# Kernel tuning notes

Measured on AMD Instinct MI355X. Metric: run time of the kernel, lower is better.

The kernel has to match this reference:

```python
import jax, jax.numpy as jnp
import numpy as np

MAX_NUM_CAPS = 10
NEG = -1e9

def _layernorm(x, g, b):
    m = x.mean(-1, keepdims=True)
    v = x.var(-1, keepdims=True)
    return (x - m) / jnp.sqrt(v + 1e-5) * g + b

def _gatv2(x, Wl, Wr, att, bias, adj):
    # x: [B,M,F]; Wl/Wr: [F,H*C]; att: [H,C]; adj: [B,M,M] bool, adj[b,i,j] = edge i->j
    B, M, F = x.shape
    H, C = att.shape
    xl = jnp.einsum('bmf,fhc->bmhc', x, Wl.reshape(F, H, C))  # source transform
    xr = jnp.einsum('bmf,fhc->bmhc', x, Wr.reshape(F, H, C))  # target transform
    # GATv2 score: att . leaky_relu(xl[i] + xr[j]) for edge (src=i, dst=j)
    z = jax.nn.leaky_relu(xl[:, :, None, :, :] + xr[:, None, :, :, :], 0.2)  # [B,i,j,H,C]
    e = jnp.einsum('bijhc,hc->bijh', z, att)
    e = jnp.where(adj[..., None], e, NEG)
    alpha = jax.nn.softmax(e, axis=1)  # softmax over incoming sources i per target j
    out = jnp.einsum('bijh,bihc->bjhc', alpha, xl)  # aggregate at targets
    return out.reshape(B, M, H * C) + bias

def setup_inputs() -> dict:
    key = jax.random.key(0)
    ks = jax.random.split(key, 16)
    B, N, T = 128, 16, 48
    Fm, H, C3 = 128, 4, 64
    s = 0.05
    inp = {
        'team_obs': jax.random.normal(ks[0], (B, N, 14), jnp.float32),
        'target_obs': jax.random.normal(ks[1], (B, T, 15), jnp.float32),
        'team_mask': jax.random.normal(ks[2], (B, 2, N), jnp.float32),
        'local_target_mask': jnp.ones((B, T + 1), jnp.float32),
        'W_emb': jax.random.normal(ks[3], (16, Fm), jnp.float32) * s,
        'b_emb': jnp.zeros((Fm,), jnp.float32),
        'Wl1': jax.random.normal(ks[4], (Fm, Fm), jnp.float32) * s,
        'Wr1': jax.random.normal(ks[5], (Fm, Fm), jnp.float32) * s,
        'att1': jax.random.normal(ks[6], (H, Fm // H), jnp.float32) * s,
        'b1': jnp.zeros((Fm,), jnp.float32),
        'Wl2': jax.random.normal(ks[7], (Fm, Fm), jnp.float32) * s,
        'Wr2': jax.random.normal(ks[8], (Fm, Fm), jnp.float32) * s,
        'att2': jax.random.normal(ks[9], (H, Fm // H), jnp.float32) * s,
        'b2': jnp.zeros((Fm,), jnp.float32),
        'Wl3': jax.random.normal(ks[10], (Fm, C3), jnp.float32) * s,
        'Wr3': jax.random.normal(ks[11], (Fm, C3), jnp.float32) * s,
        'att3': jax.random.normal(ks[12], (1, C3), jnp.float32) * s,
        'b3': jnp.zeros((C3,), jnp.float32),
        'ln1_g': jnp.ones((Fm,), jnp.float32),
        'ln1_b': jnp.zeros((Fm,), jnp.float32),
        'ln2_g': jnp.ones((Fm,), jnp.float32),
        'ln2_b': jnp.zeros((Fm,), jnp.float32),
    }
    return inp

def reference(team_obs, target_obs, team_mask, local_target_mask,
              W_emb, b_emb, Wl1, Wr1, att1, b1, Wl2, Wr2, att2, b2,
              Wl3, Wr3, att3, b3, ln1_g, ln1_b, ln2_g, ln2_b):
    B, N, _ = team_obs.shape
    team = jnp.concatenate([team_obs, jnp.zeros((B, N, 2), team_obs.dtype)], axis=2)
    tgt = target_obs[:, :, :-1]
    T = tgt.shape[1]
    tgt = jnp.concatenate([tgt[:, :, :2 + MAX_NUM_CAPS],
                           jnp.zeros((B, T, 2), tgt.dtype),
                           tgt[:, :, -2:]], axis=2)
    fin = jnp.concatenate([team, tgt], axis=1)  # [B, M, inp_dim]
    h = fin @ W_emb + b_emb  # [B, M, 128]
    imp_team = team_mask[:, 0] != -1e9          # [B, N]
    imp_tgt = local_target_mask[:, :-1] != 0.0  # [B, T]
    imp = jnp.concatenate([imp_team, imp_tgt], axis=1)  # [B, M]
    M = N + T
    eye = jnp.eye(M, dtype=bool)
    # edges among active nodes minus diagonal; PyG GATv2Conv add_self_loops=True re-adds self edges
    adj = (imp[:, :, None] & imp[:, None, :] & ~eye) | eye  # [B, M, M]
    out = jax.nn.relu(_layernorm(_gatv2(h, Wl1, Wr1, att1, b1, adj), ln1_g, ln1_b))
    out = jax.nn.relu(_layernorm(_gatv2(out, Wl2, Wr2, att2, b2, adj), ln2_g, ln2_b))
    out = _gatv2(out, Wl3, Wr3, att3, b3, adj)
    return out  # [B, M, out_dim]
```

## Files before the change

### kernel.cpp

```cpp
#include <hip/hip_runtime.h>

typedef unsigned short u16;
typedef unsigned int   u32;
typedef _Float16 h2  __attribute__((ext_vector_type(2)));
typedef __fp16   hw2 __attribute__((ext_vector_type(2)));
typedef __fp16   hw8 __attribute__((ext_vector_type(8)));
typedef float    f4  __attribute__((ext_vector_type(4)));

#define XS 136

static __device__ __forceinline__ h2 pk(float a, float b) {
    return __builtin_bit_cast(h2, __builtin_amdgcn_cvt_pkrtz(a, b));
}
static __device__ __forceinline__ float dot2(h2 a, h2 b, float c) {
    return __builtin_amdgcn_fdot2(__builtin_bit_cast(hw2, a),
                                  __builtin_bit_cast(hw2, b), c, false);
}
static __device__ __forceinline__ h2  b2h(u32 v) { return __builtin_bit_cast(h2, v); }
static __device__ __forceinline__ u32 h2u(h2 v)  { return __builtin_bit_cast(u32, v); }
static __device__ __forceinline__ h2  abs2(h2 v) { return b2h(h2u(v) & 0x7fff7fffu); }
static __device__ __forceinline__ u16 f2h(float f) { return __builtin_bit_cast(u16, (_Float16)f); }
static __device__ __forceinline__ float h2f(u16 v) { return (float)__builtin_bit_cast(_Float16, v); }
static __device__ __forceinline__ f4 mfma16(uint4 a, uint4 b, f4 c) {
    return __builtin_amdgcn_mfma_f32_16x16x32_f16(__builtin_bit_cast(hw8, a),
                                                  __builtin_bit_cast(hw8, b), c, 0, 0, 0);
}

__global__ void pack_weights(const float* __restrict__ Wl1, const float* __restrict__ Wr1,
                             const float* __restrict__ Wl2, const float* __restrict__ Wr2,
                             const float* __restrict__ Wl3, const float* __restrict__ Wr3,
                             u32* __restrict__ wpk)
{
    const int o = blockIdx.x * 256 + threadIdx.x;
    const float* src; u32* dst; int local; int N;
    if      (o < 8192)  { src = Wl1; dst = wpk;         local = o;         N = 128; }
    else if (o < 16384) { src = Wr1; dst = wpk + 8192;  local = o - 8192;  N = 128; }
    else if (o < 24576) { src = Wl2; dst = wpk + 16384; local = o - 16384; N = 128; }
    else if (o < 32768) { src = Wr2; dst = wpk + 24576; local = o - 24576; N = 128; }
    else if (o < 36864) { src = Wl3; dst = wpk + 32768; local = o - 32768; N = 64;  }
    else                { src = Wr3; dst = wpk + 36864; local = o - 36864; N = 64;  }
    const int i2   = local & 3;
    const int lane = (local >> 2) & 63;
    const int frag = local >> 8;
    const int kb   = frag & 3;
    const int nt   = frag >> 2;
    const int k0   = kb*32 + ((lane >> 4) << 3) + i2*2;
    const int n    = nt*16 + (lane & 15);
    dst[local] = h2u(pk(src[k0*N + n], src[(k0+1)*N + n]));
}

static __device__ __forceinline__ void compute_imp(int t, int b,
    const float* __restrict__ team_mask, const float* __restrict__ ltm, float* sImp)
{
    if (t < 64) {
        float im;
        if (t < 16) im = (team_mask[b*32 + t] != -1000000000.0f) ? 1.f : 0.f;
        else        im = (ltm[b*49 + (t-16)] != 0.0f) ? 1.f : 0.f;
        sImp[t] = im;
    }
}

static __device__ __forceinline__ void matmul128(int w, int lane,
    const u32* __restrict__ wpkL, const u32* __restrict__ wpkR,
    const u16* sX, u16* sXl, uint4* sXrP)
{
    const int  mt  = w & 3;
    const bool isR = (w >= 4);
    const u32* wp  = isR ? wpkR : wpkL;
    const int  n15 = lane & 15;
    const int  qd  = lane >> 4;
    uint4 afr[4];
#pragma unroll
    for (int kb = 0; kb < 4; kb++)
        afr[kb] = *(const uint4*)&sX[(mt*16 + n15)*XS + kb*32 + (qd << 3)];
#pragma unroll
    for (int nt = 0; nt < 8; nt++) {
        f4 acc = {0.f, 0.f, 0.f, 0.f};
#pragma unroll
        for (int kb = 0; kb < 4; kb++) {
            uint4 bf = *(const uint4*)&wp[((nt*4 + kb)*64 + lane)*4];
            acc = mfma16(afr[kb], bf, acc);
        }
        const int n  = nt*16 + n15;
        const int mb = mt*16 + (qd << 2);
        if (!isR) {
#pragma unroll
            for (int r = 0; r < 4; r++) sXl[(mb + r)*XS + n] = f2h(acc[r]);
        } else {
            u16* xp = (u16*)sXrP;
#pragma unroll
            for (int r = 0; r < 4; r++)
                xp[(((n >> 3)*64) + mb + r)*8 + (n & 7)] = f2h(acc[r]);
        }
    }
}

static __device__ __forceinline__ void attn_ln_fused(int w, int lane,
    const float* __restrict__ att, const float* __restrict__ bias,
    const float* __restrict__ lg, const float* __restrict__ lb,
    u16* sXout, const u16* sXl, const uint4* sXrP,
    float* sAl, float* sPart, float* sL2, const float* sImp, u32* sOv)
{
    const int h  = w & 3;
    const int hf = w >> 2;
    const int j  = lane;

    h2 a2[16];
#pragma unroll
    for (int q = 0; q < 16; q++) a2[q] = pk(att[h*32 + 2*q], att[h*32 + 2*q + 1]);

    if (w < 4) {
        const uint4* pr = (const uint4*)&sXl[lane*XS + h*32];
        float al = 0.f;
#pragma unroll
        for (int c4 = 0; c4 < 4; c4++) {
            uint4 v = pr[c4];
            al = dot2(b2h(v.x), a2[c4*4+0], al);
            al = dot2(b2h(v.y), a2[c4*4+1], al);
            al = dot2(b2h(v.z), a2[c4*4+2], al);
            al = dot2(b2h(v.w), a2[c4*4+3], al);
        }
        sAl[h*64 + lane] = al;
    }

    h2 xr2[16];
#pragma unroll
    for (int s = 0; s < 4; s++) {
        uint4 v = sXrP[(h*4 + s)*64 + j];
        xr2[s*4+0] = b2h(v.x); xr2[s*4+1] = b2h(v.y);
        xr2[s*4+2] = b2h(v.z); xr2[s*4+3] = b2h(v.w);
    }
    float Ar = 0.f;
#pragma unroll
    for (int q = 0; q < 16; q++) Ar = dot2(a2[q], xr2[q], Ar);
    const float impj = sImp[j];
    __syncthreads();

    float l = 0.f;
    h2 acc2[16];
#pragma unroll
    for (int q = 0; q < 16; q++) acc2[q] = b2h(0u);
    const int i0 = hf*32;
#pragma unroll 4
    for (int ii = 0; ii < 32; ii++) {
        const int i = i0 + ii;
        const uint4* pl = (const uint4*)&sXl[i*XS + h*32];
        uint4 v0 = pl[0], v1 = pl[1], v2 = pl[2], v3 = pl[3];
        h2 xl2[16];
        xl2[0] = b2h(v0.x); xl2[1] = b2h(v0.y); xl2[2]  = b2h(v0.z); xl2[3]  = b2h(v0.w);
        xl2[4] = b2h(v1.x); xl2[5] = b2h(v1.y); xl2[6]  = b2h(v1.z); xl2[7]  = b2h(v1.w);
        xl2[8] = b2h(v2.x); xl2[9] = b2h(v2.y); xl2[10] = b2h(v2.z); xl2[11] = b2h(v2.w);
        xl2[12]= b2h(v3.x); xl2[13]= b2h(v3.y); xl2[14] = b2h(v3.z); xl2[15] = b2h(v3.w);
        float S0 = 0.f, S1 = 0.f;
#pragma unroll
        for (int q = 0; q < 16; q += 2) {
            h2 t0 = abs2(xl2[q]   + xr2[q]);
            h2 t1 = abs2(xl2[q+1] + xr2[q+1]);
            S0 = dot2(a2[q],   t0, S0);
            S1 = dot2(a2[q+1], t1, S1);
        }
        float e  = 0.6f*(sAl[h*64 + i] + Ar) + 0.4f*(S0 + S1);
        float ad = (i == j) ? 1.f : impj * sImp[i];
        float p  = (ad != 0.f) ? __expf(e) : 0.f;
        l += p;
        h2 p2 = pk(p, p);
#pragma unroll
        for (int q = 0; q < 16; q++) acc2[q] += p2 * xl2[q];
    }

    if (hf == 1) {
        uint4* d4 = (uint4*)(sOv + (h*64 + j)*20);
        uint4 o;
        o.x = h2u(acc2[0]);  o.y = h2u(acc2[1]);  o.z = h2u(acc2[2]);  o.w = h2u(acc2[3]);  d4[0] = o;
        o.x = h2u(acc2[4]);  o.y = h2u(acc2[5]);  o.z = h2u(acc2[6]);  o.w = h2u(acc2[7]);  d4[1] = o;
        o.x = h2u(acc2[8]);  o.y = h2u(acc2[9]);  o.z = h2u(acc2[10]); o.w = h2u(acc2[11]); d4[2] = o;
        o.x = h2u(acc2[12]); o.y = h2u(acc2[13]); o.z = h2u(acc2[14]); o.w = h2u(acc2[15]); d4[3] = o;
        sL2[h*64 + j] = l;
    }
    __syncthreads();

    float yv[32];
    if (hf == 0) {
        const uint4* s4 = (const uint4*)(sOv + (h*64 + j)*20);
        uint4 u0 = s4[0], u1 = s4[1], u2 = s4[2], u3 = s4[3];
        h2 oth[16];
        oth[0] = b2h(u0.x); oth[1] = b2h(u0.y); oth[2]  = b2h(u0.z); oth[3]  = b2h(u0.w);
        oth[4] = b2h(u1.x); oth[5] = b2h(u1.y); oth[6]  = b2h(u1.z); oth[7]  = b2h(u1.w);
        oth[8] = b2h(u2.x); oth[9] = b2h(u2.y); oth[10] = b2h(u2.z); oth[11] = b2h(u2.w);
        oth[12]= b2h(u3.x); oth[13]= b2h(u3.y); oth[14] = b2h(u3.z); oth[15] = b2h(u3.w);
        l += sL2[h*64 + j];
        const float rl = 1.f / l;
        float s1 = 0.f, s2v = 0.f;
#pragma unroll
        for (int q = 0; q < 16; q++) {
            h2 sum = acc2[q] + oth[q];
            float y0 = fmaf((float)sum[0], rl, bias[h*32 + 2*q]);
            float y1 = fmaf((float)sum[1], rl, bias[h*32 + 2*q + 1]);
            yv[2*q] = y0; yv[2*q+1] = y1;
            s1 += y0 + y1;
            s2v = fmaf(y0, y0, s2v);
            s2v = fmaf(y1, y1, s2v);
        }
        sPart[h*64 + j]       = s1;
        sPart[256 + h*64 + j] = s2v;
    }
    __syncthreads();

    if (hf == 0) {
        float su = sPart[j] + sPart[64 + j] + sPart[128 + j] + sPart[192 + j];
        float sq = sPart[256 + j] + sPart[320 + j] + sPart[384 + j] + sPart[448 + j];
        const float mean = su * 0.0078125f;
        const float var  = sq * 0.0078125f - mean*mean;
        const float rstd = rsqrtf(var + 1e-5f);
        u32 orow[16];
#pragma unroll
        for (int q = 0; q < 16; q++) {
            int f0 = h*32 + 2*q;
            float v0 = fmaxf(fmaf((yv[2*q]   - mean)*rstd, lg[f0],   lb[f0]),   0.f);
            float v1 = fmaxf(fmaf((yv[2*q+1] - mean)*rstd, lg[f0+1], lb[f0+1]), 0.f);
            orow[q] = h2u(pk(v0, v1));
        }
        uint4* po = (uint4*)&sXout[j*XS + h*32];
        po[0] = *(uint4*)&orow[0];
        po[1] = *(uint4*)&orow[4];
        po[2] = *(uint4*)&orow[8];
        po[3] = *(uint4*)&orow[12];
    }
}

__global__ void __launch_bounds__(512, 1) gnn_fused(
    const float* __restrict__ team_obs, const float* __restrict__ target_obs,
    const float* __restrict__ team_mask, const float* __restrict__ ltm,
    const float* __restrict__ W_emb, const float* __restrict__ b_emb,
    const float* __restrict__ att1, const float* __restrict__ b1,
    const float* __restrict__ ln1_g, const float* __restrict__ ln1_b,
    const float* __restrict__ att2, const float* __restrict__ b2,
    const float* __restrict__ ln2_g, const float* __restrict__ ln2_b,
    const float* __restrict__ att3, const float* __restrict__ b3,
    const u32* __restrict__ wpk, float* __restrict__ out)
{
    __shared__ __align__(16) u16   sX  [64*XS];
    __shared__ __align__(16) u16   sXl [64*XS];
    __shared__ __align__(16) uint4 sXrP[1024];
    __shared__ float sFin[1024];
    __shared__ float sAl [256];
    __shared__ float sPart[512];
    __shared__ float sL2 [256];
    __shared__ float sImp[64];
    __shared__ __align__(16) u32 sOv[5120];

    const int t    = threadIdx.x;
    const int w    = t >> 6;
    const int lane = t & 63;
    const int b    = blockIdx.x;

    compute_imp(t, b, team_mask, ltm, sImp);
    for (int ee = t; ee < 1024; ee += 512) {
        int m = ee >> 4, k = ee & 15;
        float v = 0.f;
        if (m < 16) {
            if (k < 14) v = team_obs[(b*16 + m)*14 + k];
        } else {
            const float* tg = target_obs + (size_t)(b*48 + (m-16))*15;
            if      (k < 12)  v = tg[k];
            else if (k == 14) v = tg[12];
            else if (k == 15) v = tg[13];
        }
        sFin[m*16 + k] = v;
    }
    __syncthreads();

    {
        const int f = t & 127;
        const int g = t >> 7;
        float wreg[16];
#pragma unroll
        for (int k = 0; k < 16; k++) wreg[k] = W_emb[k*128 + f];
        const float bf = b_emb[f];
#pragma unroll
        for (int mm = 0; mm < 16; mm++) {
            int m = g*16 + mm;
            const float4* pf = (const float4*)&sFin[m*16];
            float4 f0 = pf[0], f1 = pf[1], f2 = pf[2], f3 = pf[3];
            float acc = bf;
            acc = fmaf(f0.x, wreg[0],  acc); acc = fmaf(f0.y, wreg[1],  acc);
            acc = fmaf(f0.z, wreg[2],  acc); acc = fmaf(f0.w, wreg[3],  acc);
            acc = fmaf(f1.x, wreg[4],  acc); acc = fmaf(f1.y, wreg[5],  acc);
            acc = fmaf(f1.z, wreg[6],  acc); acc = fmaf(f1.w, wreg[7],  acc);
            acc = fmaf(f2.x, wreg[8],  acc); acc = fmaf(f2.y, wreg[9],  acc);
            acc = fmaf(f2.z, wreg[10], acc); acc = fmaf(f2.w, wreg[11], acc);
            acc = fmaf(f3.x, wreg[12], acc); acc = fmaf(f3.y, wreg[13], acc);
            acc = fmaf(f3.z, wreg[14], acc); acc = fmaf(f3.w, wreg[15], acc);
            sX[m*XS + f] = f2h(acc);
        }
    }
    __syncthreads();

    matmul128(w, lane, wpk, wpk + 8192, sX, sXl, sXrP);
    __syncthreads();
    attn_ln_fused(w, lane, att1, b1, ln1_g, ln1_b,
                  sX, sXl, sXrP, sAl, sPart, sL2, sImp, sOv);
    __syncthreads();

    matmul128(w, lane, wpk + 16384, wpk + 24576, sX, sXl, sXrP);
    __syncthreads();
    attn_ln_fused(w, lane, att2, b2, ln2_g, ln2_b,
                  sX, sXl, sXrP, sAl, sPart, sL2, sImp, sOv);
    __syncthreads();

    {
        const int  mt  = w & 3;
        const bool isR = (w >= 4);
        const u32* wp  = isR ? (wpk + 36864) : (wpk + 32768);
        const int  n15 = lane & 15;
        const int  qd  = lane >> 4;
        uint4 afr[4];
#pragma unroll
        for (int kb = 0; kb < 4; kb++)
            afr[kb] = *(const uint4*)&sX[(mt*16 + n15)*XS + kb*32 + (qd << 3)];
#pragma unroll
        for (int nt = 0; nt < 4; nt++) {
            f4 acc = {0.f, 0.f, 0.f, 0.f};
#pragma unroll
            for (int kb = 0; kb < 4; kb++) {
                uint4 bf = *(const uint4*)&wp[((nt*4 + kb)*64 + lane)*4];
                acc = mfma16(afr[kb], bf, acc);
            }
            const int n  = nt*16 + n15;
            const int mb = mt*16 + (qd << 2);
            if (!isR) {
#pragma unroll
                for (int r = 0; r < 4; r++) sXl[(mb + r)*XS + n] = f2h(acc[r]);
            } else {
                u16* xp = (u16*)sXrP;
#pragma unroll
                for (int r = 0; r < 4; r++)
                    xp[(((n >> 3)*64) + mb + r)*8 + (n & 7)] = f2h(acc[r]);
            }
        }
    }
    __syncthreads();

    {
        h2 a2l[4];
#pragma unroll
        for (int q = 0; q < 4; q++) a2l[q] = pk(att3[w*8 + 2*q], att3[w*8 + 2*q + 1]);
        uint4 v = *(const uint4*)&sXl[lane*XS + w*8];
        float al = 0.f;
        al = dot2(b2h(v.x), a2l[0], al);
        al = dot2(b2h(v.y), a2l[1], al);
        al = dot2(b2h(v.z), a2l[2], al);
        al = dot2(b2h(v.w), a2l[3], al);
        sPart[w*64 + lane] = al;
    }
    __syncthreads();
    if (t < 64) {
        sAl[t] = ((sPart[t] + sPart[64+t]) + (sPart[128+t] + sPart[192+t]))
               + ((sPart[256+t] + sPart[320+t]) + (sPart[384+t] + sPart[448+t]));
    }
    __syncthreads();

    u16* sE = (u16*)sOv;

    {
        h2 a3[32], xr3[32];
#pragma unroll
        for (int q = 0; q < 32; q++) a3[q] = pk(att3[2*q], att3[2*q + 1]);
#pragma unroll
        for (int s = 0; s < 8; s++) {
            uint4 v = sXrP[s*64 + lane];
            xr3[s*4+0] = b2h(v.x); xr3[s*4+1] = b2h(v.y);
            xr3[s*4+2] = b2h(v.z); xr3[s*4+3] = b2h(v.w);
        }
        float Ar = 0.f;
#pragma unroll
        for (int q = 0; q < 32; q++) Ar = dot2(a3[q], xr3[q], Ar);
        const float impj = sImp[lane];
#pragma unroll
        for (int ii = 0; ii < 8; ii++) {
            const int i = w*8 + ii;
            const uint4* pl = (const uint4*)&sXl[i*XS];
            float S0 = 0.f, S1 = 0.f;
#pragma unroll
            for (int c4 = 0; c4 < 8; c4++) {
                uint4 v = pl[c4];
                S0 = dot2(a3[c4*4+0], abs2(b2h(v.x) + xr3[c4*4+0]), S0);
                S1 = dot2(a3[c4*4+1], abs2(b2h(v.y) + xr3[c4*4+1]), S1);
                S0 = dot2(a3[c4*4+2], abs2(b2h(v.z) + xr3[c4*4+2]), S0);
                S1 = dot2(a3[c4*4+3], abs2(b2h(v.w) + xr3[c4*4+3]), S1);
            }
            float e  = 0.6f*(sAl[i] + Ar) + 0.4f*(S0 + S1);
            float ad = (i == lane) ? 1.f : impj * sImp[i];
            e = (ad != 0.f) ? e : -60000.0f;
            sE[i*64 + lane] = f2h(e);
        }
    }
    __syncthreads();

    {
        const int c0 = w*8;
        h2 acc2[4];
#pragma unroll
        for (int q = 0; q < 4; q++) acc2[q] = b2h(0u);
        float l = 0.f;
        for (int i = 0; i < 64; i++) {
            float p = __expf(h2f(sE[i*64 + lane]));
            l += p;
            h2 p2 = pk(p, p);
            uint4 v = *(const uint4*)&sXl[i*XS + c0];
            acc2[0] += p2 * b2h(v.x);
            acc2[1] += p2 * b2h(v.y);
            acc2[2] += p2 * b2h(v.z);
            acc2[3] += p2 * b2h(v.w);
        }
        const float rl = 1.f / l;
        float o[8];
#pragma unroll
        for (int q = 0; q < 4; q++) {
            o[2*q]   = fmaf((float)acc2[q][0], rl, b3[c0 + 2*q]);
            o[2*q+1] = fmaf((float)acc2[q][1], rl, b3[c0 + 2*q + 1]);
        }
        float4* po = (float4*)(out + (size_t)b*4096 + (size_t)lane*64 + c0);
        po[0] = *(const float4*)&o[0];
        po[1] = *(const float4*)&o[4];
    }
}

extern "C" void kernel_launch(void* const* d_in, const int* in_sizes, int n_in,
                              void* d_out, int out_size, void* d_ws, size_t ws_size,
                              hipStream_t stream) {
    (void)in_sizes; (void)n_in; (void)ws_size; (void)out_size;
    const float* team_obs          = (const float*)d_in[0];
    const float* target_obs        = (const float*)d_in[1];
    const float* team_mask         = (const float*)d_in[2];
    const float* local_target_mask = (const float*)d_in[3];
    const float* W_emb             = (const float*)d_in[4];
    const float* b_emb             = (const float*)d_in[5];
    const float* Wl1               = (const float*)d_in[6];
    const float* Wr1               = (const float*)d_in[7];
    const float* att1              = (const float*)d_in[8];
    const float* b1                = (const float*)d_in[9];
    const float* Wl2               = (const float*)d_in[10];
    const float* Wr2               = (const float*)d_in[11];
    const float* att2              = (const float*)d_in[12];
    const float* b2                = (const float*)d_in[13];
    const float* Wl3               = (const float*)d_in[14];
    const float* Wr3               = (const float*)d_in[15];
    const float* att3              = (const float*)d_in[16];
    const float* b3                = (const float*)d_in[17];
    const float* ln1_g             = (const float*)d_in[18];
    const float* ln1_b             = (const float*)d_in[19];
    const float* ln2_g             = (const float*)d_in[20];
    const float* ln2_b             = (const float*)d_in[21];
    float* out = (float*)d_out;

    u32* wpk = (u32*)d_ws;

    pack_weights<<<dim3(160), dim3(256), 0, stream>>>(Wl1, Wr1, Wl2, Wr2, Wl3, Wr3, wpk);
    gnn_fused<<<dim3(128), dim3(512), 0, stream>>>(
        team_obs, target_obs, team_mask, local_target_mask, W_emb, b_emb,
        att1, b1, ln1_g, ln1_b, att2, b2, ln2_g, ln2_b, att3, b3, wpk, out);
}
```

Before: 146.4 us.

## Double block to 1024 threads and split every stage across 16 waves

The fused GNN kernel now launches 1024 threads per block instead of 512, and each stage splits its work across 16 waves. Matmul N-tiles are halved per wave, the attention source loop is split into four quarters with a three-way shared-memory reduction, and the layer-3 stages use 4 columns per wave. With only 128 blocks on a GPU with many CUs, the aim is more latency hiding per CU. In exchange it uses more shared memory for the partial sums, adds reduction overhead, accumulates in fp32 rather than fp16 when combining partials, and lowers the register budget per thread.

```diff
diff --git a/kernel.cpp b/kernel.cpp
--- a/kernel.cpp
+++ b/kernel.cpp
@@ -65,7 +65,8 @@
     const u16* sX, u16* sXl, uint4* sXrP)
 {
     const int  mt  = w & 3;
-    const bool isR = (w >= 4);
+    const bool isR = (w >> 2) & 1;
+    const int  nh  = w >> 3;
     const u32* wp  = isR ? wpkR : wpkL;
     const int  n15 = lane & 15;
     const int  qd  = lane >> 4;
@@ -74,7 +75,7 @@
     for (int kb = 0; kb < 4; kb++)
         afr[kb] = *(const uint4*)&sX[(mt*16 + n15)*XS + kb*32 + (qd << 3)];
 #pragma unroll
-    for (int nt = 0; nt < 8; nt++) {
+    for (int nt = nh*4; nt < nh*4 + 4; nt++) {
         f4 acc = {0.f, 0.f, 0.f, 0.f};
 #pragma unroll
         for (int kb = 0; kb < 4; kb++) {
@@ -102,7 +103,7 @@
     float* sAl, float* sPart, float* sL2, const float* sImp, u32* sOv)
 {
     const int h  = w & 3;
-    const int hf = w >> 2;
+    const int qf = w >> 2;
     const int j  = lane;
 
     h2 a2[16];
@@ -140,9 +141,9 @@
     h2 acc2[16];
 #pragma unroll
     for (int q = 0; q < 16; q++) acc2[q] = b2h(0u);
-    const int i0 = hf*32;
+    const int i0 = qf*16;
 #pragma unroll 4
-    for (int ii = 0; ii < 32; ii++) {
+    for (int ii = 0; ii < 16; ii++) {
         const int i = i0 + ii;
         const uint4* pl = (const uint4*)&sXl[i*XS + h*32];
         uint4 v0 = pl[0], v1 = pl[1], v2 = pl[2], v3 = pl[3];
@@ -168,45 +169,53 @@
         for (int q = 0; q < 16; q++) acc2[q] += p2 * xl2[q];
     }
 
-    if (hf == 1) {
-        uint4* d4 = (uint4*)(sOv + (h*64 + j)*20);
+    if (qf != 0) {
+        uint4* d4 = (uint4*)(sOv + ((qf-1)*256 + h*64 + j)*20);
         uint4 o;
         o.x = h2u(acc2[0]);  o.y = h2u(acc2[1]);  o.z = h2u(acc2[2]);  o.w = h2u(acc2[3]);  d4[0] = o;
         o.x = h2u(acc2[4]);  o.y = h2u(acc2[5]);  o.z = h2u(acc2[6]);  o.w = h2u(acc2[7]);  d4[1] = o;
         o.x = h2u(acc2[8]);  o.y = h2u(acc2[9]);  o.z = h2u(acc2[10]); o.w = h2u(acc2[11]); d4[2] = o;
         o.x = h2u(acc2[12]); o.y = h2u(acc2[13]); o.z = h2u(acc2[14]); o.w = h2u(acc2[15]); d4[3] = o;
-        sL2[h*64 + j] = l;
-    }
-    __syncthreads();
-
-    float yv[32];
-    if (hf == 0) {
-        const uint4* s4 = (const uint4*)(sOv + (h*64 + j)*20);
-        uint4 u0 = s4[0], u1 = s4[1], u2 = s4[2], u3 = s4[3];
-        h2 oth[16];
-        oth[0] = b2h(u0.x); oth[1] = b2h(u0.y); oth[2]  = b2h(u0.z); oth[3]  = b2h(u0.w);
-        oth[4] = b2h(u1.x); oth[5] = b2h(u1.y); oth[6]  = b2h(u1.z); oth[7]  = b2h(u1.w);
-        oth[8] = b2h(u2.x); oth[9] = b2h(u2.y); oth[10] = b2h(u2.z); oth[11] = b2h(u2.w);
-        oth[12]= b2h(u3.x); oth[13]= b2h(u3.y); oth[14] = b2h(u3.z); oth[15] = b2h(u3.w);
-        l += sL2[h*64 + j];
+        sL2[(qf-1)*256 + h*64 + j] = l;
+    }
+    __syncthreads();
+
+    float fy[32];
+    if (qf == 0) {
+#pragma unroll
+        for (int q = 0; q < 16; q++) {
+            fy[2*q]   = (float)acc2[q][0];
+            fy[2*q+1] = (float)acc2[q][1];
+        }
+#pragma unroll
+        for (int bb = 0; bb < 3; bb++) {
+            const uint4* s4 = (const uint4*)(sOv + (bb*256 + h*64 + j)*20);
+            uint4 U[4];
+            U[0] = s4[0]; U[1] = s4[1]; U[2] = s4[2]; U[3] = s4[3];
+            const u32* uv = (const u32*)U;
+#pragma unroll
+            for (int q = 0; q < 16; q++) {
+                h2 o = b2h(uv[q]);
+                fy[2*q]   += (float)o[0];
+                fy[2*q+1] += (float)o[1];
+            }
+            l += sL2[bb*256 + h*64 + j];
+        }
         const float rl = 1.f / l;
         float s1 = 0.f, s2v = 0.f;
 #pragma unroll
-        for (int q = 0; q < 16; q++) {
-            h2 sum = acc2[q] + oth[q];
-            float y0 = fmaf((float)sum[0], rl, bias[h*32 + 2*q]);
-            float y1 = fmaf((float)sum[1], rl, bias[h*32 + 2*q + 1]);
-            yv[2*q] = y0; yv[2*q+1] = y1;
-            s1 += y0 + y1;
-            s2v = fmaf(y0, y0, s2v);
-            s2v = fmaf(y1, y1, s2v);
+        for (int k = 0; k < 32; k++) {
+            float y = fmaf(fy[k], rl, bias[h*32 + k]);
+            fy[k] = y;
+            s1  += y;
+            s2v  = fmaf(y, y, s2v);
         }
         sPart[h*64 + j]       = s1;
         sPart[256 + h*64 + j] = s2v;
     }
     __syncthreads();
 
-    if (hf == 0) {
+    if (qf == 0) {
         float su = sPart[j] + sPart[64 + j] + sPart[128 + j] + sPart[192 + j];
         float sq = sPart[256 + j] + sPart[320 + j] + sPart[384 + j] + sPart[448 + j];
         const float mean = su * 0.0078125f;
@@ -216,8 +225,8 @@
 #pragma unroll
         for (int q = 0; q < 16; q++) {
             int f0 = h*32 + 2*q;
-            float v0 = fmaxf(fmaf((yv[2*q]   - mean)*rstd, lg[f0],   lb[f0]),   0.f);
-            float v1 = fmaxf(fmaf((yv[2*q+1] - mean)*rstd, lg[f0+1], lb[f0+1]), 0.f);
+            float v0 = fmaxf(fmaf((fy[2*q]   - mean)*rstd, lg[f0],   lb[f0]),   0.f);
+            float v1 = fmaxf(fmaf((fy[2*q+1] - mean)*rstd, lg[f0+1], lb[f0+1]), 0.f);
             orow[q] = h2u(pk(v0, v1));
         }
         uint4* po = (uint4*)&sXout[j*XS + h*32];
@@ -228,7 +237,7 @@
     }
 }
 
-__global__ void __launch_bounds__(512, 1) gnn_fused(
+__global__ void __launch_bounds__(1024, 1) gnn_fused(
     const float* __restrict__ team_obs, const float* __restrict__ target_obs,
     const float* __restrict__ team_mask, const float* __restrict__ ltm,
     const float* __restrict__ W_emb, const float* __restrict__ b_emb,
@@ -244,10 +253,10 @@
     __shared__ __align__(16) uint4 sXrP[1024];
     __shared__ float sFin[1024];
     __shared__ float sAl [256];
-    __shared__ float sPart[512];
-    __shared__ float sL2 [256];
+    __shared__ float sPart[1024];
+    __shared__ float sL2 [768];
     __shared__ float sImp[64];
-    __shared__ __align__(16) u32 sOv[5120];
+    __shared__ __align__(16) u32 sOv[15360];
 
     const int t    = threadIdx.x;
     const int w    = t >> 6;
@@ -255,8 +264,8 @@
     const int b    = blockIdx.x;
 
     compute_imp(t, b, team_mask, ltm, sImp);
-    for (int ee = t; ee < 1024; ee += 512) {
-        int m = ee >> 4, k = ee & 15;
+    {
+        int m = t >> 4, k = t & 15;
         float v = 0.f;
         if (m < 16) {
             if (k < 14) v = team_obs[(b*16 + m)*14 + k];
@@ -278,8 +287,8 @@
         for (int k = 0; k < 16; k++) wreg[k] = W_emb[k*128 + f];
         const float bf = b_emb[f];
 #pragma unroll
-        for (int mm = 0; mm < 16; mm++) {
-            int m = g*16 + mm;
+        for (int mm = 0; mm < 8; mm++) {
+            int m = g*8 + mm;
             const float4* pf = (const float4*)&sFin[m*16];
             float4 f0 = pf[0], f1 = pf[1], f2 = pf[2], f3 = pf[3];
             float acc = bf;
@@ -310,7 +319,8 @@
 
     {
         const int  mt  = w & 3;
-        const bool isR = (w >= 4);
+        const bool isR = (w >> 2) & 1;
+        const int  nh  = w >> 3;
         const u32* wp  = isR ? (wpk + 36864) : (wpk + 32768);
         const int  n15 = lane & 15;
         const int  qd  = lane >> 4;
@@ -319,7 +329,7 @@
         for (int kb = 0; kb < 4; kb++)
             afr[kb] = *(const uint4*)&sX[(mt*16 + n15)*XS + kb*32 + (qd << 3)];
 #pragma unroll
-        for (int nt = 0; nt < 4; nt++) {
+        for (int nt = nh*2; nt < nh*2 + 2; nt++) {
             f4 acc = {0.f, 0.f, 0.f, 0.f};
 #pragma unroll
             for (int kb = 0; kb < 4; kb++) {
@@ -342,21 +352,22 @@
     __syncthreads();
 
     {
-        h2 a2l[4];
-#pragma unroll
-        for (int q = 0; q < 4; q++) a2l[q] = pk(att3[w*8 + 2*q], att3[w*8 + 2*q + 1]);
-        uint4 v = *(const uint4*)&sXl[lane*XS + w*8];
-        float al = 0.f;
-        al = dot2(b2h(v.x), a2l[0], al);
+        h2 a2l[2];
+        a2l[0] = pk(att3[w*4 + 0], att3[w*4 + 1]);
+        a2l[1] = pk(att3[w*4 + 2], att3[w*4 + 3]);
+        uint2 v = *(const uint2*)&sXl[lane*XS + w*4];
+        float al = dot2(b2h(v.x), a2l[0], 0.f);
         al = dot2(b2h(v.y), a2l[1], al);
-        al = dot2(b2h(v.z), a2l[2], al);
-        al = dot2(b2h(v.w), a2l[3], al);
         sPart[w*64 + lane] = al;
     }
     __syncthreads();
     if (t < 64) {
-        sAl[t] = ((sPart[t] + sPart[64+t]) + (sPart[128+t] + sPart[192+t]))
-               + ((sPart[256+t] + sPart[320+t]) + (sPart[384+t] + sPart[448+t]));
+        float s = 0.f;
+#pragma unroll
+        for (int p = 0; p < 16; p += 4)
+            s += ((sPart[p*64 + t] + sPart[(p+1)*64 + t]) +
+                  (sPart[(p+2)*64 + t] + sPart[(p+3)*64 + t]));
+        sAl[t] = s;
     }
     __syncthreads();
 
@@ -377,8 +388,8 @@
         for (int q = 0; q < 32; q++) Ar = dot2(a3[q], xr3[q], Ar);
         const float impj = sImp[lane];
 #pragma unroll
-        for (int ii = 0; ii < 8; ii++) {
-            const int i = w*8 + ii;
+        for (int ii = 0; ii < 4; ii++) {
+            const int i = w*4 + ii;
             const uint4* pl = (const uint4*)&sXl[i*XS];
             float S0 = 0.f, S1 = 0.f;
 #pragma unroll
@@ -398,31 +409,25 @@
     __syncthreads();
 
     {
-        const int c0 = w*8;
-        h2 acc2[4];
-#pragma unroll
-        for (int q = 0; q < 4; q++) acc2[q] = b2h(0u);
+        const int c0 = w*4;
+        h2 acc2[2];
+        acc2[0] = b2h(0u); acc2[1] = b2h(0u);
         float l = 0.f;
         for (int i = 0; i < 64; i++) {
             float p = __expf(h2f(sE[i*64 + lane]));
             l += p;
             h2 p2 = pk(p, p);
-            uint4 v = *(const uint4*)&sXl[i*XS + c0];
+            uint2 v = *(const uint2*)&sXl[i*XS + c0];
             acc2[0] += p2 * b2h(v.x);
             acc2[1] += p2 * b2h(v.y);
-            acc2[2] += p2 * b2h(v.z);
-            acc2[3] += p2 * b2h(v.w);
         }
         const float rl = 1.f / l;
-        float o[8];
-#pragma unroll
-        for (int q = 0; q < 4; q++) {
-            o[2*q]   = fmaf((float)acc2[q][0], rl, b3[c0 + 2*q]);
-            o[2*q+1] = fmaf((float)acc2[q][1], rl, b3[c0 + 2*q + 1]);
-        }
-        float4* po = (float4*)(out + (size_t)b*4096 + (size_t)lane*64 + c0);
-        po[0] = *(const float4*)&o[0];
-        po[1] = *(const float4*)&o[4];
+        float4 o4;
+        o4.x = fmaf((float)acc2[0][0], rl, b3[c0 + 0]);
+        o4.y = fmaf((float)acc2[0][1], rl, b3[c0 + 1]);
+        o4.z = fmaf((float)acc2[1][0], rl, b3[c0 + 2]);
+        o4.w = fmaf((float)acc2[1][1], rl, b3[c0 + 3]);
+        *(float4*)(out + (size_t)b*4096 + (size_t)lane*64 + c0) = o4;
     }
 }
 
@@ -457,7 +462,7 @@
     u32* wpk = (u32*)d_ws;
 
     pack_weights<<<dim3(160), dim3(256), 0, stream>>>(Wl1, Wr1, Wl2, Wr2, Wl3, Wr3, wpk);
-    gnn_fused<<<dim3(128), dim3(512), 0, stream>>>(
+    gnn_fused<<<dim3(128), dim3(1024), 0, stream>>>(
         team_obs, target_obs, team_mask, local_target_mask, W_emb, b_emb,
         att1, b1, ln1_g, ln1_b, att2, b2, ln2_g, ln2_b, att3, b3, wpk, out);
 }
```

Result: slower. 156.0 us (+6.6%).

## Split GATv2 attention into score and MFMA aggregation phases

Applied to the files above, without the earlier changes.

The fused attention loop now only computes unnormalized softmax weights, which are stored as fp16 into a new shared buffer. The alpha·xl aggregation becomes MFMA 16x16x32 matmuls against a transposed copy of xl, which the projection matmul now also writes. The same change is applied to layer 3, replacing the scalar loop that re-evaluated exp over stored scores. It adds more shared memory (a larger P buffer, a transposed xl and an fp32 output staging buffer) and extra barriers. This may lower occupancy.

```diff
diff --git a/kernel.cpp b/kernel.cpp
--- a/kernel.cpp
+++ b/kernel.cpp
@@ -8,6 +8,9 @@
 typedef float    f4  __attribute__((ext_vector_type(4)));
 
 #define XS 136
+#define PS 72
+#define BS 72
+#define OS 72
 
 static __device__ __forceinline__ h2 pk(float a, float b) {
     return __builtin_bit_cast(h2, __builtin_amdgcn_cvt_pkrtz(a, b));
@@ -20,7 +23,6 @@
 static __device__ __forceinline__ u32 h2u(h2 v)  { return __builtin_bit_cast(u32, v); }
 static __device__ __forceinline__ h2  abs2(h2 v) { return b2h(h2u(v) & 0x7fff7fffu); }
 static __device__ __forceinline__ u16 f2h(float f) { return __builtin_bit_cast(u16, (_Float16)f); }
-static __device__ __forceinline__ float h2f(u16 v) { return (float)__builtin_bit_cast(_Float16, v); }
 static __device__ __forceinline__ f4 mfma16(uint4 a, uint4 b, f4 c) {
     return __builtin_amdgcn_mfma_f32_16x16x32_f16(__builtin_bit_cast(hw8, a),
                                                   __builtin_bit_cast(hw8, b), c, 0, 0, 0);
@@ -62,7 +64,7 @@
 
 static __device__ __forceinline__ void matmul128(int w, int lane,
     const u32* __restrict__ wpkL, const u32* __restrict__ wpkR,
-    const u16* sX, u16* sXl, uint4* sXrP)
+    const u16* sX, u16* sXl, uint4* sXrP, u16* sXlB)
 {
     const int  mt  = w & 3;
     const bool isR = (w >= 4);
@@ -86,6 +88,10 @@
         if (!isR) {
 #pragma unroll
             for (int r = 0; r < 4; r++) sXl[(mb + r)*XS + n] = f2h(acc[r]);
+            uint2 u;
+            u.x = h2u(pk(acc[0], acc[1]));
+            u.y = h2u(pk(acc[2], acc[3]));
+            *(uint2*)&sXlB[n*BS + mb] = u;
         } else {
             u16* xp = (u16*)sXrP;
 #pragma unroll
@@ -95,11 +101,10 @@
     }
 }
 
-static __device__ __forceinline__ void attn_ln_fused(int w, int lane,
-    const float* __restrict__ att, const float* __restrict__ bias,
-    const float* __restrict__ lg, const float* __restrict__ lb,
-    u16* sXout, const u16* sXl, const uint4* sXrP,
-    float* sAl, float* sPart, float* sL2, const float* sImp, u32* sOv)
+static __device__ __forceinline__ void attn_scores(int w, int lane,
+    const float* __restrict__ att,
+    const u16* sXl, const uint4* sXrP, u16* sP,
+    float* sAl, float* sL2, const float* sImp)
 {
     const int h  = w & 3;
     const int hf = w >> 2;
@@ -137,94 +142,104 @@
     __syncthreads();
 
     float l = 0.f;
-    h2 acc2[16];
-#pragma unroll
-    for (int q = 0; q < 16; q++) acc2[q] = b2h(0u);
-    const int i0 = hf*32;
-#pragma unroll 4
-    for (int ii = 0; ii < 32; ii++) {
-        const int i = i0 + ii;
-        const uint4* pl = (const uint4*)&sXl[i*XS + h*32];
-        uint4 v0 = pl[0], v1 = pl[1], v2 = pl[2], v3 = pl[3];
-        h2 xl2[16];
-        xl2[0] = b2h(v0.x); xl2[1] = b2h(v0.y); xl2[2]  = b2h(v0.z); xl2[3]  = b2h(v0.w);
-        xl2[4] = b2h(v1.x); xl2[5] = b2h(v1.y); xl2[6]  = b2h(v1.z); xl2[7]  = b2h(v1.w);
-        xl2[8] = b2h(v2.x); xl2[9] = b2h(v2.y); xl2[10] = b2h(v2.z); xl2[11] = b2h(v2.w);
-        xl2[12]= b2h(v3.x); xl2[13]= b2h(v3.y); xl2[14] = b2h(v3.z); xl2[15] = b2h(v3.w);
-        float S0 = 0.f, S1 = 0.f;
-#pragma unroll
-        for (int q = 0; q < 16; q += 2) {
-            h2 t0 = abs2(xl2[q]   + xr2[q]);
-            h2 t1 = abs2(xl2[q+1] + xr2[q+1]);
-            S0 = dot2(a2[q],   t0, S0);
-            S1 = dot2(a2[q+1], t1, S1);
-        }
-        float e  = 0.6f*(sAl[h*64 + i] + Ar) + 0.4f*(S0 + S1);
-        float ad = (i == j) ? 1.f : impj * sImp[i];
-        float p  = (ad != 0.f) ? __expf(e) : 0.f;
-        l += p;
-        h2 p2 = pk(p, p);
-#pragma unroll
-        for (int q = 0; q < 16; q++) acc2[q] += p2 * xl2[q];
-    }
-
-    if (hf == 1) {
-        uint4* d4 = (uint4*)(sOv + (h*64 + j)*20);
-        uint4 o;
-        o.x = h2u(acc2[0]);  o.y = h2u(acc2[1]);  o.z = h2u(acc2[2]);  o.w = h2u(acc2[3]);  d4[0] = o;
-        o.x = h2u(acc2[4]);  o.y = h2u(acc2[5]);  o.z = h2u(acc2[6]);  o.w = h2u(acc2[7]);  d4[1] = o;
-        o.x = h2u(acc2[8]);  o.y = h2u(acc2[9]);  o.z = h2u(acc2[10]); o.w = h2u(acc2[11]); d4[2] = o;
-        o.x = h2u(acc2[12]); o.y = h2u(acc2[13]); o.z = h2u(acc2[14]); o.w = h2u(acc2[15]); d4[3] = o;
-        sL2[h*64 + j] = l;
-    }
-    __syncthreads();
-
-    float yv[32];
-    if (hf == 0) {
-        const uint4* s4 = (const uint4*)(sOv + (h*64 + j)*20);
-        uint4 u0 = s4[0], u1 = s4[1], u2 = s4[2], u3 = s4[3];
-        h2 oth[16];
-        oth[0] = b2h(u0.x); oth[1] = b2h(u0.y); oth[2]  = b2h(u0.z); oth[3]  = b2h(u0.w);
-        oth[4] = b2h(u1.x); oth[5] = b2h(u1.y); oth[6]  = b2h(u1.z); oth[7]  = b2h(u1.w);
-        oth[8] = b2h(u2.x); oth[9] = b2h(u2.y); oth[10] = b2h(u2.z); oth[11] = b2h(u2.w);
-        oth[12]= b2h(u3.x); oth[13]= b2h(u3.y); oth[14] = b2h(u3.z); oth[15] = b2h(u3.w);
-        l += sL2[h*64 + j];
-        const float rl = 1.f / l;
-        float s1 = 0.f, s2v = 0.f;
-#pragma unroll
-        for (int q = 0; q < 16; q++) {
-            h2 sum = acc2[q] + oth[q];
-            float y0 = fmaf((float)sum[0], rl, bias[h*32 + 2*q]);
-            float y1 = fmaf((float)sum[1], rl, bias[h*32 + 2*q + 1]);
-            yv[2*q] = y0; yv[2*q+1] = y1;
-            s1 += y0 + y1;
-            s2v = fmaf(y0, y0, s2v);
-            s2v = fmaf(y1, y1, s2v);
-        }
-        sPart[h*64 + j]       = s1;
-        sPart[256 + h*64 + j] = s2v;
-    }
-    __syncthreads();
-
-    if (hf == 0) {
-        float su = sPart[j] + sPart[64 + j] + sPart[128 + j] + sPart[192 + j];
-        float sq = sPart[256 + j] + sPart[320 + j] + sPart[384 + j] + sPart[448 + j];
-        const float mean = su * 0.0078125f;
-        const float var  = sq * 0.0078125f - mean*mean;
-        const float rstd = rsqrtf(var + 1e-5f);
-        u32 orow[16];
-#pragma unroll
-        for (int q = 0; q < 16; q++) {
-            int f0 = h*32 + 2*q;
-            float v0 = fmaxf(fmaf((yv[2*q]   - mean)*rstd, lg[f0],   lb[f0]),   0.f);
-            float v1 = fmaxf(fmaf((yv[2*q+1] - mean)*rstd, lg[f0+1], lb[f0+1]), 0.f);
-            orow[q] = h2u(pk(v0, v1));
-        }
-        uint4* po = (uint4*)&sXout[j*XS + h*32];
-        po[0] = *(uint4*)&orow[0];
-        po[1] = *(uint4*)&orow[4];
-        po[2] = *(uint4*)&orow[8];
-        po[3] = *(uint4*)&orow[12];
+    uint4* pd = (uint4*)&sP[(h*64 + j)*PS + hf*32];
+    for (int c8 = 0; c8 < 4; c8++) {
+        u32 pr4[4];
+        float pprev = 0.f;
+#pragma unroll
+        for (int i2 = 0; i2 < 8; i2++) {
+            const int i = hf*32 + c8*8 + i2;
+            const uint4* pl = (const uint4*)&sXl[i*XS + h*32];
+            uint4 v0 = pl[0], v1 = pl[1], v2 = pl[2], v3 = pl[3];
+            h2 xl2[16];
+            xl2[0] = b2h(v0.x); xl2[1] = b2h(v0.y); xl2[2]  = b2h(v0.z); xl2[3]  = b2h(v0.w);
+            xl2[4] = b2h(v1.x); xl2[5] = b2h(v1.y); xl2[6]  = b2h(v1.z); xl2[7]  = b2h(v1.w);
+            xl2[8] = b2h(v2.x); xl2[9] = b2h(v2.y); xl2[10] = b2h(v2.z); xl2[11] = b2h(v2.w);
+            xl2[12]= b2h(v3.x); xl2[13]= b2h(v3.y); xl2[14] = b2h(v3.z); xl2[15] = b2h(v3.w);
+            float S0 = 0.f, S1 = 0.f;
+#pragma unroll
+            for (int q = 0; q < 16; q += 2) {
+                h2 t0 = abs2(xl2[q]   + xr2[q]);
+                h2 t1 = abs2(xl2[q+1] + xr2[q+1]);
+                S0 = dot2(a2[q],   t0, S0);
+                S1 = dot2(a2[q+1], t1, S1);
+            }
+            float e  = 0.6f*(sAl[h*64 + i] + Ar) + 0.4f*(S0 + S1);
+            float ad = (i == j) ? 1.f : impj * sImp[i];
+            float p  = (ad != 0.f) ? __expf(e) : 0.f;
+            if (i2 & 1) {
+                h2 pp = pk(pprev, p);
+                pr4[i2 >> 1] = h2u(pp);
+                l += (float)pp[0] + (float)pp[1];
+            } else {
+                pprev = p;
+            }
+        }
+        pd[c8] = make_uint4(pr4[0], pr4[1], pr4[2], pr4[3]);
+    }
+    sL2[h*128 + hf*64 + j] = l;
+}
+
+static __device__ __forceinline__ void attn_agg_ln(int w, int lane,
+    const float* __restrict__ bias, const float* __restrict__ lg, const float* __restrict__ lb,
+    const u16* sP, const u16* sXlB, float* sOutF, const float* sL2,
+    float* sPart, u16* sXout)
+{
+    const int h   = w & 3;
+    const int jh2 = w >> 2;
+    const int n15 = lane & 15;
+    const int kq  = lane >> 4;
+
+    f4 acc00 = {0.f,0.f,0.f,0.f}, acc01 = acc00, acc10 = acc00, acc11 = acc00;
+#pragma unroll
+    for (int ks = 0; ks < 2; ks++) {
+        uint4 af0 = *(const uint4*)&sP[(h*64 + (jh2*2+0)*16 + n15)*PS + ks*32 + kq*8];
+        uint4 af1 = *(const uint4*)&sP[(h*64 + (jh2*2+1)*16 + n15)*PS + ks*32 + kq*8];
+        uint4 bf0 = *(const uint4*)&sXlB[(h*32 +  0 + n15)*BS + ks*32 + kq*8];
+        uint4 bf1 = *(const uint4*)&sXlB[(h*32 + 16 + n15)*BS + ks*32 + kq*8];
+        acc00 = mfma16(af0, bf0, acc00);
+        acc01 = mfma16(af0, bf1, acc01);
+        acc10 = mfma16(af1, bf0, acc10);
+        acc11 = mfma16(af1, bf1, acc11);
+    }
+    {
+        const int jb0 = jh2*32 + kq*4;
+#pragma unroll
+        for (int r = 0; r < 4; r++) {
+            sOutF[(h*32 +  0 + n15)*OS + jb0 + r]      = acc00[r];
+            sOutF[(h*32 + 16 + n15)*OS + jb0 + r]      = acc01[r];
+            sOutF[(h*32 +  0 + n15)*OS + jb0 + 16 + r] = acc10[r];
+            sOutF[(h*32 + 16 + n15)*OS + jb0 + 16 + r] = acc11[r];
+        }
+    }
+    __syncthreads();
+
+    const int cg = w, j = lane, hh = w >> 1;
+    const float l  = sL2[hh*128 + j] + sL2[hh*128 + 64 + j];
+    const float rl = 1.f / l;
+    float y[16];
+    float s1 = 0.f, s2 = 0.f;
+#pragma unroll
+    for (int k = 0; k < 16; k++) {
+        float v = fmaf(sOutF[(cg*16 + k)*OS + j], rl, bias[cg*16 + k]);
+        y[k] = v; s1 += v; s2 = fmaf(v, v, s2);
+    }
+    sPart[cg*64 + j] = s1;
+    sPart[512 + cg*64 + j] = s2;
+    __syncthreads();
+    float su = 0.f, sq = 0.f;
+#pragma unroll
+    for (int p = 0; p < 8; p++) { su += sPart[p*64 + j]; sq += sPart[512 + p*64 + j]; }
+    const float mean = su * 0.0078125f;
+    const float var  = sq * 0.0078125f - mean*mean;
+    const float rstd = rsqrtf(var + 1e-5f);
+    u32* xo = (u32*)&sXout[j*XS];
+#pragma unroll
+    for (int q = 0; q < 8; q++) {
+        const int c0 = cg*16 + 2*q;
+        float v0 = fmaxf(fmaf((y[2*q]   - mean)*rstd, lg[c0],   lb[c0]),   0.f);
+        float v1 = fmaxf(fmaf((y[2*q+1] - mean)*rstd, lg[c0+1], lb[c0+1]), 0.f);
+        xo[cg*8 + q] = h2u(pk(v0, v1));
     }
 }
 
@@ -242,17 +257,20 @@
     __shared__ __align__(16) u16   sX  [64*XS];
     __shared__ __align__(16) u16   sXl [64*XS];
     __shared__ __align__(16) uint4 sXrP[1024];
-    __shared__ float sFin[1024];
+    __shared__ __align__(16) u16   sXlB[128*BS];
+    __shared__ __align__(16) u16   sP  [4*64*PS];
+    __shared__ __align__(16) float sOutF[128*OS];
     __shared__ float sAl [256];
-    __shared__ float sPart[512];
-    __shared__ float sL2 [256];
+    __shared__ float sPart[1024];
+    __shared__ float sL2 [768];
     __shared__ float sImp[64];
-    __shared__ __align__(16) u32 sOv[5120];
 
     const int t    = threadIdx.x;
     const int w    = t >> 6;
     const int lane = t & 63;
     const int b    = blockIdx.x;
+
+    float* sFin = (float*)sP;
 
     compute_imp(t, b, team_mask, ltm, sImp);
     for (int ee = t; ee < 1024; ee += 512) {
@@ -296,16 +314,18 @@
     }
     __syncthreads();
 
-    matmul128(w, lane, wpk, wpk + 8192, sX, sXl, sXrP);
-    __syncthreads();
-    attn_ln_fused(w, lane, att1, b1, ln1_g, ln1_b,
-                  sX, sXl, sXrP, sAl, sPart, sL2, sImp, sOv);
-    __syncthreads();
-
-    matmul128(w, lane, wpk + 16384, wpk + 24576, sX, sXl, sXrP);
-    __syncthreads();
-    attn_ln_fused(w, lane, att2, b2, ln2_g, ln2_b,
-                  sX, sXl, sXrP, sAl, sPart, sL2, sImp, sOv);
+    matmul128(w, lane, wpk, wpk + 8192, sX, sXl, sXrP, sXlB);
+    __syncthreads();
+    attn_scores(w, lane, att1, sXl, sXrP, sP, sAl, sL2, sImp);
+    __syncthreads();
+    attn_agg_ln(w, lane, b1, ln1_g, ln1_b, sP, sXlB, sOutF, sL2, sPart, sX);
+    __syncthreads();
+
+    matmul128(w, lane, wpk + 16384, wpk + 24576, sX, sXl, sXrP, sXlB);
+    __syncthreads();
+    attn_scores(w, lane, att2, sXl, sXrP, sP, sAl, sL2, sImp);
+    __syncthreads();
+    attn_agg_ln(w, lane, b2, ln2_g, ln2_b, sP, sXlB, sOutF, sL2, sPart, sX);
     __syncthreads();
 
     {
@@ -331,6 +351,10 @@
             if (!isR) {
 #pragma unroll
                 for (int r = 0; r < 4; r++) sXl[(mb + r)*XS + n] = f2h(acc[r]);
+                uint2 u;
+                u.x = h2u(pk(acc[0], acc[1]));
+                u.y = h2u(pk(acc[2], acc[3]));
+                *(uint2*)&sXlB[n*BS + mb] = u;
             } else {
                 u16* xp = (u16*)sXrP;
 #pragma unroll
@@ -360,8 +384,6 @@
     }
     __syncthreads();
 
-    u16* sE = (u16*)sOv;
-
     {
         h2 a3[32], xr3[32];
 #pragma unroll
@@ -376,6 +398,9 @@
 #pragma unroll
         for (int q = 0; q < 32; q++) Ar = dot2(a3[q], xr3[q], Ar);
         const float impj = sImp[lane];
+        float l3 = 0.f;
+        u32 pr4[4];
+        float pprev = 0.f;
 #pragma unroll
         for (int ii = 0; ii < 8; ii++) {
             const int i = w*8 + ii;
@@ -391,38 +416,50 @@
             }
             float e  = 0.6f*(sAl[i] + Ar) + 0.4f*(S0 + S1);
             float ad = (i == lane) ? 1.f : impj * sImp[i];
-            e = (ad != 0.f) ? e : -60000.0f;
-            sE[i*64 + lane] = f2h(e);
-        }
-    }
-    __syncthreads();
+            float p  = (ad != 0.f) ? __expf(e) : 0.f;
+            if (ii & 1) {
+                h2 pp = pk(pprev, p);
+                pr4[ii >> 1] = h2u(pp);
+                l3 += (float)pp[0] + (float)pp[1];
+            } else {
+                pprev = p;
+            }
+        }
+        *(uint4*)&sP[lane*PS + w*8] = make_uint4(pr4[0], pr4[1], pr4[2], pr4[3]);
+        sPart[w*64 + lane] = l3;
+    }
+    __syncthreads();
+    if (t < 64) {
+        float s = ((sPart[t] + sPart[64+t]) + (sPart[128+t] + sPart[192+t]))
+                + ((sPart[256+t] + sPart[320+t]) + (sPart[384+t] + sPart[448+t]));
+        sL2[t] = 1.f / s;
+    }
 
     {
-        const int c0 = w*8;
-        h2 acc2[4];
-#pragma unroll
-        for (int q = 0; q < 4; q++) acc2[q] = b2h(0u);
-        float l = 0.f;
-        for (int i = 0; i < 64; i++) {
-            float p = __expf(h2f(sE[i*64 + lane]));
-            l += p;
-            h2 p2 = pk(p, p);
-            uint4 v = *(const uint4*)&sXl[i*XS + c0];
-            acc2[0] += p2 * b2h(v.x);
-            acc2[1] += p2 * b2h(v.y);
-            acc2[2] += p2 * b2h(v.z);
-            acc2[3] += p2 * b2h(v.w);
-        }
-        const float rl = 1.f / l;
-        float o[8];
-#pragma unroll
-        for (int q = 0; q < 4; q++) {
-            o[2*q]   = fmaf((float)acc2[q][0], rl, b3[c0 + 2*q]);
-            o[2*q+1] = fmaf((float)acc2[q][1], rl, b3[c0 + 2*q + 1]);
-        }
-        float4* po = (float4*)(out + (size_t)b*4096 + (size_t)lane*64 + c0);
-        po[0] = *(const float4*)&o[0];
-        po[1] = *(const float4*)&o[4];
+        const int jt  = w & 3;
+        const int cth = w >> 2;
+        const int n15 = lane & 15;
+        const int kq  = lane >> 4;
+        f4 acc0 = {0.f,0.f,0.f,0.f}, acc1 = acc0;
+#pragma unroll
+        for (int ks = 0; ks < 2; ks++) {
+            uint4 af = *(const uint4*)&sP[(jt*16 + n15)*PS + ks*32 + kq*8];
+            uint4 bf0 = *(const uint4*)&sXlB[((cth*2+0)*16 + n15)*BS + ks*32 + kq*8];
+            uint4 bf1 = *(const uint4*)&sXlB[((cth*2+1)*16 + n15)*BS + ks*32 + kq*8];
+            acc0 = mfma16(af, bf0, acc0);
+            acc1 = mfma16(af, bf1, acc1);
+        }
+        __syncthreads();
+        const int c0 = (cth*2+0)*16 + n15;
+        const int c1 = (cth*2+1)*16 + n15;
+        const float bc0 = b3[c0], bc1 = b3[c1];
+#pragma unroll
+        for (int r = 0; r < 4; r++) {
+            const int jj = jt*16 + kq*4 + r;
+            const float rl = sL2[jj];
+            out[(size_t)b*4096 + (size_t)jj*64 + c0] = fmaf(acc0[r], rl, bc0);
+            out[(size_t)b*4096 + (size_t)jj*64 + c1] = fmaf(acc1[r], rl, bc1);
+        }
     }
 }
 
```

Result: faster. 143.3 us (-2.1%).
